# Performance work log

Hardware: AMD Instinct MI355X
Metric: run time of the kernel (lower is better)

Reference implementation:

```python
import jax, jax.numpy as jnp
import numpy as np

HEADS = 16
DIM_HEAD = 64
NPATCH = 256
LN_EPS = 1e-5


def setup_inputs() -> dict:
    key = jax.random.key(0)
    ks = jax.random.split(key, 6)
    B, S, D = 4, 2048, 1024
    inner = HEADS * DIM_HEAD  # 1024
    x = jax.random.normal(ks[0], (B, S, D), dtype=jnp.float32)
    ln_gamma = jnp.ones((D,), dtype=jnp.float32)
    ln_beta = jnp.zeros((D,), dtype=jnp.float32)
    # torch Linear: y = x @ W.T; we store the transposed weight directly.
    Wqkv = jax.random.normal(ks[1], (D, 3 * inner), dtype=jnp.float32) / np.sqrt(D)
    Wout = jax.random.normal(ks[2], (inner, D), dtype=jnp.float32) / np.sqrt(inner)
    bout = jnp.zeros((D,), dtype=jnp.float32)
    return {"x": x, "ln_gamma": ln_gamma, "ln_beta": ln_beta,
            "Wqkv": Wqkv, "Wout": Wout, "bout": bout}


def reference(x, ln_gamma, ln_beta, Wqkv, Wout, bout):
    B, S, D = x.shape
    # LayerNorm
    mu = jnp.mean(x, axis=-1, keepdims=True)
    var = jnp.mean(jnp.square(x - mu), axis=-1, keepdims=True)
    xn = (x - mu) * jax.lax.rsqrt(var + LN_EPS) * ln_gamma + ln_beta
    # QKV projection
    qkv = xn @ Wqkv  # [B, S, 3*H*Dh]
    q, k, v = jnp.split(qkv, 3, axis=-1)
    q = q.reshape(B, S, HEADS, DIM_HEAD)
    k = k.reshape(B, S, HEADS, DIM_HEAD)
    v = v.reshape(B, S, HEADS, DIM_HEAD)
    scale = DIM_HEAD ** -0.5
    dots = jnp.einsum('bqhd,bkhd->bhqk', q, k) * scale  # [B,H,S,S]
    # block-causal mask: query window i attends to key windows 0..i
    win = jnp.arange(S) // NPATCH
    mask = win[:, None] >= win[None, :]  # [S, S] bool
    dots = jnp.where(mask[None, None], dots, -jnp.inf)
    attn = jax.nn.softmax(dots, axis=-1)
    out = jnp.einsum('bhqk,bkhd->bqhd', attn, v).reshape(B, S, HEADS * DIM_HEAD)
    return out @ Wout + bout
```

## Files before the change

### kernel.cpp

```cpp
#include <hip/hip_runtime.h>
#include <stdint.h>

typedef unsigned short u16;
typedef __attribute__((ext_vector_type(8))) short bf16x8;
typedef __attribute__((ext_vector_type(4))) float f32x4;
typedef __attribute__((ext_vector_type(4))) unsigned short u16x4;
typedef __attribute__((ext_vector_type(4))) unsigned int u32x4;

#define DEVI static __device__ __forceinline__

#define QSCALE (0.125f * 1.4426950408889634f)

DEVI u16 f2bf(float f) {
  union { float f; unsigned int u; } v; v.f = f;
  unsigned int u = v.u + 0x7fffu + ((v.u >> 16) & 1u);
  return (u16)(u >> 16);
}
DEVI void gl16(const void* g, void* l) {
  __builtin_amdgcn_global_load_lds(
      (__attribute__((address_space(1))) void*)g,
      (__attribute__((address_space(3))) void*)l, 16, 0, 0);
}
DEVI unsigned int cvtpk(float a, float b) {
  unsigned int r;
  asm("v_cvt_pk_bf16_f32 %0, %1, %2" : "=v"(r) : "v"(a), "v"(b));
  return r;
}
DEVI float fexp2(float x) {
  float r;
  asm("v_exp_f32 %0, %1\n\ts_nop 0" : "=v"(r) : "v"(x));
  return r;
}
DEVI float fmax4(f32x4 v) {
  return fmaxf(fmaxf(v[0], v[1]), fmaxf(v[2], v[3]));
}

__global__ __launch_bounds__(256) void k_ln_split(
    const float* __restrict__ x, const float* __restrict__ gamma,
    const float* __restrict__ beta, u16* __restrict__ xh) {
  const int row = blockIdx.x;
  const int t = threadIdx.x;
  const float4* xr = (const float4*)(x + (size_t)row * 1024);
  float4 v = xr[t];
  float s = v.x + v.y + v.z + v.w;
  float s2 = v.x * v.x + v.y * v.y + v.z * v.z + v.w * v.w;
  #pragma unroll
  for (int m = 1; m < 64; m <<= 1) { s += __shfl_xor(s, m); s2 += __shfl_xor(s2, m); }
  __shared__ float ls[4], ls2[4];
  if ((t & 63) == 0) { ls[t >> 6] = s; ls2[t >> 6] = s2; }
  __syncthreads();
  s = ls[0] + ls[1] + ls[2] + ls[3];
  s2 = ls2[0] + ls2[1] + ls2[2] + ls2[3];
  float mu = s * (1.0f / 1024.0f);
  float var = s2 * (1.0f / 1024.0f) - mu * mu;
  float rstd = rsqrtf(var + 1e-5f);
  float4 g = ((const float4*)gamma)[t];
  float4 b = ((const float4*)beta)[t];
  float xv[4] = {v.x, v.y, v.z, v.w};
  float gg[4] = {g.x, g.y, g.z, g.w};
  float bb[4] = {b.x, b.y, b.z, b.w};
  u16x4 hv;
  #pragma unroll
  for (int i = 0; i < 4; i++) {
    float xn = (xv[i] - mu) * rstd * gg[i] + bb[i];
    hv[i] = f2bf(xn);
  }
  ((u16x4*)xh)[(size_t)row * 256 + t] = hv;
}

__global__ __launch_bounds__(256) void k_wsplit_t(
    const float* __restrict__ W, u16* __restrict__ Wth, int K, int N) {
  __shared__ float tile[32][33];
  const int t = threadIdx.x;
  const int tx = t & 31, ty = t >> 5;
  #pragma unroll
  for (int i = 0; i < 4; i++) {
    int k = blockIdx.y * 32 + ty + i * 8;
    int n = blockIdx.x * 32 + tx;
    tile[ty + i * 8][tx] = W[(size_t)k * N + n];
  }
  __syncthreads();
  #pragma unroll
  for (int i = 0; i < 4; i++) {
    int n = blockIdx.x * 32 + ty + i * 8;
    int k = blockIdx.y * 32 + tx;
    Wth[(size_t)n * K + k] = f2bf(tile[tx][ty + i * 8]);
  }
}

__global__ __launch_bounds__(512, 2) void k_gemmq(
    const u16* __restrict__ Ah, const u16* __restrict__ Bh,
    u16* __restrict__ Qh, u16* __restrict__ Kh, u16* __restrict__ Vth) {
  __shared__ u16 sA[2][256 * 64];
  __shared__ u16 sB[2][256 * 64];
  const int t = threadIdx.x, lane = t & 63, w = t >> 6;
  const int bm = blockIdx.x, bn = blockIdx.y;
  const int wm2 = w >> 2, wn4 = w & 3;
  const int g = lane >> 4, c = lane & 15;
  const size_t arow0 = (size_t)bm * 256, brow0 = (size_t)bn * 256;

  const int sr = t >> 3;
  const int scs = (t & 7) ^ (sr & 7);
  const int brs = (t >> 3) & 31;
  const int bcs = (t & 7) ^ (brs & 7);
  const int bsj = t >> 8;

  f32x4 acc[8][4] = {};

#define STAGE_A(u, kt, b) do { \
    int rA0 = (u) * 64 + sr, rA1 = 128 + rA0; \
    gl16(Ah + (arow0 + rA0) * 1024 + (size_t)(kt) * 64 + scs * 8, \
         sA[b] + (size_t)((u) * 512 + t) * 8); \
    gl16(Ah + (arow0 + rA1) * 1024 + (size_t)(kt) * 64 + scs * 8, \
         sA[b] + (size_t)(1024 + (u) * 512 + t) * 8); \
  } while (0)
#define STAGE_B(u, kt, b) do { \
    int s0_ = bsj, s1_ = bsj + 2; \
    int rB0 = (u) * 32 + s0_ * 64 + brs, rB1 = (u) * 32 + s1_ * 64 + brs; \
    gl16(Bh + (brow0 + rB0) * 1024 + (size_t)(kt) * 64 + bcs * 8, \
         sB[b] + (size_t)(rB0 * 8 + (t & 7)) * 8); \
    gl16(Bh + (brow0 + rB1) * 1024 + (size_t)(kt) * 64 + bcs * 8, \
         sB[b] + (size_t)(rB1 * 8 + (t & 7)) * 8); \
  } while (0)
#define PWAIT_V(tail) do { \
    if (tail) asm volatile("s_waitcnt vmcnt(0)" ::: "memory"); \
    else      asm volatile("s_waitcnt vmcnt(6)" ::: "memory"); \
    __builtin_amdgcn_s_barrier(); \
    asm volatile("s_waitcnt lgkmcnt(0)" ::: "memory"); \
  } while (0)
#define PWAIT_N() do { \
    __builtin_amdgcn_s_barrier(); \
    asm volatile("s_waitcnt lgkmcnt(0)" ::: "memory"); \
  } while (0)

  STAGE_A(0, 0, 0); STAGE_B(0, 0, 0);
  STAGE_A(1, 0, 0); STAGE_B(1, 0, 0);
  STAGE_A(0, 1, 1); STAGE_B(0, 1, 1);
  PWAIT_V(0);

  bf16x8 af[8], bf0[4], bf1[4];
  for (int kt = 0; kt < 16; kt++) {
    const int cur = kt & 1;
    const int tail = (kt >= 14);
    const u16* A_ = sA[cur];
    const u16* B_ = sB[cur];

    #pragma unroll
    for (int mi = 0; mi < 4; mi++)
      #pragma unroll
      for (int ks = 0; ks < 2; ks++) {
        int row = wm2 * 128 + mi * 16 + c;
        af[mi * 2 + ks] = *(const bf16x8*)(A_ + row * 64 + (((ks * 4 + g) ^ (row & 7)) * 8));
      }
    #pragma unroll
    for (int ni = 0; ni < 2; ni++)
      #pragma unroll
      for (int ks = 0; ks < 2; ks++) {
        int row = wn4 * 64 + ni * 16 + c;
        bf0[ni * 2 + ks] = *(const bf16x8*)(B_ + row * 64 + (((ks * 4 + g) ^ (row & 7)) * 8));
      }
    if (kt + 1 < 16) STAGE_A(1, kt + 1, (kt + 1) & 1);
    PWAIT_V(tail);
    __builtin_amdgcn_s_setprio(1);
    #pragma unroll
    for (int mi = 0; mi < 4; mi++)
      #pragma unroll
      for (int ni = 0; ni < 2; ni++)
        #pragma unroll
        for (int ks = 0; ks < 2; ks++)
          acc[mi][ni] = __builtin_amdgcn_mfma_f32_16x16x32_bf16(af[mi * 2 + ks], bf0[ni * 2 + ks], acc[mi][ni], 0, 0, 0);
    __builtin_amdgcn_s_setprio(0);

    #pragma unroll
    for (int ni = 0; ni < 2; ni++)
      #pragma unroll
      for (int ks = 0; ks < 2; ks++) {
        int row = wn4 * 64 + 32 + ni * 16 + c;
        bf1[ni * 2 + ks] = *(const bf16x8*)(B_ + row * 64 + (((ks * 4 + g) ^ (row & 7)) * 8));
      }
    if (kt + 1 < 16) STAGE_B(1, kt + 1, (kt + 1) & 1);
    PWAIT_N();
    __builtin_amdgcn_s_setprio(1);
    #pragma unroll
    for (int mi = 0; mi < 4; mi++)
      #pragma unroll
      for (int ni = 0; ni < 2; ni++)
        #pragma unroll
        for (int ks = 0; ks < 2; ks++)
          acc[mi][2 + ni] = __builtin_amdgcn_mfma_f32_16x16x32_bf16(af[mi * 2 + ks], bf1[ni * 2 + ks], acc[mi][2 + ni], 0, 0, 0);
    __builtin_amdgcn_s_setprio(0);

    #pragma unroll
    for (int mi = 0; mi < 4; mi++)
      #pragma unroll
      for (int ks = 0; ks < 2; ks++) {
        int row = wm2 * 128 + 64 + mi * 16 + c;
        af[mi * 2 + ks] = *(const bf16x8*)(A_ + row * 64 + (((ks * 4 + g) ^ (row & 7)) * 8));
      }
    if (kt + 2 < 16) STAGE_A(0, kt + 2, cur);
    PWAIT_N();
    __builtin_amdgcn_s_setprio(1);
    #pragma unroll
    for (int mi = 0; mi < 4; mi++)
      #pragma unroll
      for (int ni = 0; ni < 2; ni++)
        #pragma unroll
        for (int ks = 0; ks < 2; ks++)
          acc[4 + mi][ni] = __builtin_amdgcn_mfma_f32_16x16x32_bf16(af[mi * 2 + ks], bf0[ni * 2 + ks], acc[4 + mi][ni], 0, 0, 0);
    __builtin_amdgcn_s_setprio(0);

    if (kt + 2 < 16) STAGE_B(0, kt + 2, cur);
    PWAIT_N();
    __builtin_amdgcn_s_setprio(1);
    #pragma unroll
    for (int mi = 0; mi < 4; mi++)
      #pragma unroll
      for (int ni = 0; ni < 2; ni++)
        #pragma unroll
        for (int ks = 0; ks < 2; ks++)
          acc[4 + mi][2 + ni] = __builtin_amdgcn_mfma_f32_16x16x32_bf16(af[mi * 2 + ks], bf1[ni * 2 + ks], acc[4 + mi][2 + ni], 0, 0, 0);
    __builtin_amdgcn_s_setprio(0);
  }

  #pragma unroll
  for (int am = 0; am < 8; am++) {
    int grow0 = bm * 256 + wm2 * 128 + (am >> 2) * 64 + (am & 3) * 16 + g * 4;
    int b = grow0 >> 11, s0 = grow0 & 2047;
    #pragma unroll
    for (int an = 0; an < 4; an++) {
      int gcol = bn * 256 + wn4 * 64 + (an >> 1) * 32 + (an & 1) * 16 + c;
      int which = gcol >> 10, rem = gcol & 1023;
      int hh = rem >> 6, dd = rem & 63;
      if (which == 2) {
        u16x4 hv;
        #pragma unroll
        for (int r = 0; r < 4; r++) hv[r] = f2bf(acc[am][an][r]);
        size_t off = ((size_t)((b * 16 + hh) * 64 + dd)) * 2048 + s0;
        *(u16x4*)(Vth + off) = hv;
      } else {
        u16* dh = which ? Kh : Qh;
        float sc = which ? 1.0f : QSCALE;
        #pragma unroll
        for (int r = 0; r < 4; r++) {
          size_t off = ((size_t)(b * 16 + hh) * 2048 + (s0 + r)) * 64 + dd;
          dh[off] = f2bf(acc[am][an][r] * sc);
        }
      }
    }
  }
#undef STAGE_A
#undef STAGE_B
#undef PWAIT_V
#undef PWAIT_N
}

__global__ __launch_bounds__(256) void k_gemmo(
    const u16* __restrict__ Ah, const u16* __restrict__ Bh,
    float* __restrict__ Cout, const float* __restrict__ bias) {
  __shared__ u16 sA[2][128 * 64];
  __shared__ u16 sB[2][128 * 64];
  const int t = threadIdx.x, lane = t & 63, w = t >> 6;
  const int bm = blockIdx.x, bn = blockIdx.y;
  const int wm = (w >> 1) * 64, wn = (w & 1) * 64;
  const int g = lane >> 4, c = lane & 15;
  const size_t arow0 = (size_t)bm * 128, brow0 = (size_t)bn * 128;

  const int r0 = t >> 3, cc0 = t & 7;
  const int cs0 = cc0 ^ (r0 & 7);
  const u16* gA = Ah + (arow0 + r0) * 1024 + cs0 * 8;
  const u16* gB = Bh + (brow0 + r0) * 1024 + cs0 * 8;

  f32x4 acc[4][4] = {};

  #pragma unroll
  for (int i = 0; i < 4; i++) {
    gl16(gA + (size_t)i * 32768, sA[0] + (size_t)(t + i * 256) * 8);
    gl16(gB + (size_t)i * 32768, sB[0] + (size_t)(t + i * 256) * 8);
  }
  gA += 64; gB += 64;
  __syncthreads();

  for (int kt = 0; kt < 16; kt++) {
    const int cur = kt & 1, nxt = cur ^ 1;
    if (kt + 1 < 16) {
      #pragma unroll
      for (int i = 0; i < 4; i++) {
        gl16(gA + (size_t)i * 32768, sA[nxt] + (size_t)(t + i * 256) * 8);
        gl16(gB + (size_t)i * 32768, sB[nxt] + (size_t)(t + i * 256) * 8);
      }
      gA += 64; gB += 64;
    }
    #pragma unroll
    for (int ks = 0; ks < 2; ks++) {
      bf16x8 afh[4], bfh[4];
      #pragma unroll
      for (int mi = 0; mi < 4; mi++) {
        int row = wm + mi * 16 + c;
        afh[mi] = *(const bf16x8*)(sA[cur] + row * 64 + (((ks * 4 + g) ^ (row & 7)) * 8));
      }
      #pragma unroll
      for (int ni = 0; ni < 4; ni++) {
        int row = wn + ni * 16 + c;
        bfh[ni] = *(const bf16x8*)(sB[cur] + row * 64 + (((ks * 4 + g) ^ (row & 7)) * 8));
      }
      #pragma unroll
      for (int mi = 0; mi < 4; mi++)
        #pragma unroll
        for (int ni = 0; ni < 4; ni++)
          acc[mi][ni] = __builtin_amdgcn_mfma_f32_16x16x32_bf16(afh[mi], bfh[ni], acc[mi][ni], 0, 0, 0);
    }
    __syncthreads();
  }

  #pragma unroll
  for (int mi = 0; mi < 4; mi++) {
    int grow0 = bm * 128 + wm + mi * 16 + g * 4;
    #pragma unroll
    for (int ni = 0; ni < 4; ni++) {
      int gcol = bn * 128 + wn + ni * 16 + c;
      float bb = bias[gcol];
      #pragma unroll
      for (int r = 0; r < 4; r++)
        Cout[(size_t)(grow0 + r) * 1024 + gcol] = acc[mi][ni][r] + bb;
    }
  }
}

__global__ __launch_bounds__(512, 4) void k_attn(
    const u16* __restrict__ Qh, const u16* __restrict__ Kh,
    const u16* __restrict__ Vth, u16* __restrict__ Oh) {
  __shared__ u16 lK[2][128 * 64], lV[2][64 * 128];
  const int t = threadIdx.x, lane = t & 63, w = t >> 6;
  const int bh = blockIdx.x;
  const int qt = 15 - blockIdx.y;
  const int b = bh >> 4, h = bh & 15;
  const int qrow0 = qt * 128;
  const int kvlen = (qt / 2 + 1) * 256;
  const int g = lane >> 4, c = lane & 15;

  bf16x8 qf[2];
  {
    const u16* qb = Qh + ((size_t)bh * 2048 + qrow0 + w * 16) * 64;
    #pragma unroll
    for (int ks = 0; ks < 2; ks++)
      qf[ks] = *(const bf16x8*)(qb + (size_t)c * 64 + ks * 32 + g * 8);
  }

  const u16* Kb = Kh + (size_t)bh * 2048 * 64;
  const u16* Vb = Vth + (size_t)bh * 64 * 2048;

  int kbase[2], vbase[4];
  #pragma unroll
  for (int ks = 0; ks < 2; ks++) kbase[ks] = c * 64 + (((ks * 4 + g) ^ (c & 7)) * 8);
  #pragma unroll
  for (int ks = 0; ks < 4; ks++) vbase[ks] = c * 128 + (((ks * 4 + g) ^ c) * 8);

  const int kr0 = t >> 3, kcs0 = (t & 7) ^ (kr0 & 7);
  const int vr0 = t >> 4, vcs0 = (t & 15) ^ (vr0 & 15);

  const bf16x8 vones = {(short)0x3F80, (short)0x3F80, (short)0x3F80, (short)0x3F80,
                        (short)0x3F80, (short)0x3F80, (short)0x3F80, (short)0x3F80};

  float mrun = 0.f;
  f32x4 lsum = {0.f, 0.f, 0.f, 0.f};
  f32x4 o[4] = {};

  const int ntiles = kvlen >> 7;

  gl16(Kb + (size_t)kr0 * 64 + kcs0 * 8, lK[0] + (size_t)t * 8);
  gl16(Kb + (size_t)(kr0 + 64) * 64 + kcs0 * 8, lK[0] + (size_t)(t + 512) * 8);
  gl16(Vb + (size_t)vr0 * 2048 + vcs0 * 8, lV[0] + (size_t)t * 8);
  gl16(Vb + (size_t)(vr0 + 32) * 2048 + vcs0 * 8, lV[0] + (size_t)(t + 512) * 8);
  __syncthreads();

  const u16* gK = Kb + (size_t)(128 + kr0) * 64 + kcs0 * 8;
  const u16* gV = Vb + (size_t)vr0 * 2048 + 128 + vcs0 * 8;

  for (int kt = 0; kt < ntiles; kt++) {
    const int cur = kt & 1, nxt = cur ^ 1;
    if (kt + 1 < ntiles) {
      gl16(gK, lK[nxt] + (size_t)t * 8);
      gl16(gK + 64 * 64, lK[nxt] + (size_t)(t + 512) * 8);
      gl16(gV, lV[nxt] + (size_t)t * 8);
      gl16(gV + 32 * 2048, lV[nxt] + (size_t)(t + 512) * 8);
      gK += 128 * 64;  gV += 128;
    }

    f32x4 s[8];
    #pragma unroll
    for (int ni = 0; ni < 8; ni++)
      s[ni] = (f32x4){-mrun, -mrun, -mrun, -mrun};
    __builtin_amdgcn_s_setprio(1);
    #pragma unroll
    for (int ni = 0; ni < 8; ni++)
      #pragma unroll
      for (int ks = 0; ks < 2; ks++) {
        bf16x8 kf = *(const bf16x8*)(lK[cur] + ni * 1024 + kbase[ks]);
        s[ni] = __builtin_amdgcn_mfma_f32_16x16x32_bf16(kf, qf[ks], s[ni], 0, 0, 0);
      }
    __builtin_amdgcn_s_setprio(0);

    float tl = fmaxf(fmaxf(fmaxf(fmax4(s[0]), fmax4(s[1])), fmaxf(fmax4(s[2]), fmax4(s[3]))),
                     fmaxf(fmaxf(fmax4(s[4]), fmax4(s[5])), fmaxf(fmax4(s[6]), fmax4(s[7]))));
    if (!__all(tl <= 8.0f)) {
      float tm = fmaxf(tl, __shfl_xor(tl, 16));
      tm = fmaxf(tm, __shfl_xor(tm, 32));
      float delta = fmaxf(tm, 0.0f);
      mrun += delta;
      float al = fexp2(-delta);
      #pragma unroll
      for (int ni = 0; ni < 8; ni++)
        #pragma unroll
        for (int r = 0; r < 4; r++) s[ni][r] -= delta;
      #pragma unroll
      for (int r = 0; r < 4; r++) {
        float ar = __shfl(al, g * 4 + r);
        lsum[r] *= ar;
        #pragma unroll
        for (int di = 0; di < 4; di++) o[di][r] *= ar;
      }
    }

    bf16x8 pa[4];
    #pragma unroll
    for (int ks = 0; ks < 4; ks++) {
      unsigned int e0 = cvtpk(fexp2(s[2 * ks][0]), fexp2(s[2 * ks][1]));
      unsigned int e1 = cvtpk(fexp2(s[2 * ks][2]), fexp2(s[2 * ks][3]));
      unsigned int f0 = cvtpk(fexp2(s[2 * ks + 1][0]), fexp2(s[2 * ks + 1][1]));
      unsigned int f1 = cvtpk(fexp2(s[2 * ks + 1][2]), fexp2(s[2 * ks + 1][3]));
      asm volatile("v_permlane32_swap_b32 %0, %1" : "+v"(e0), "+v"(f0));
      asm volatile("v_permlane16_swap_b32 %0, %1" : "+v"(e0), "+v"(f0));
      asm volatile("v_permlane32_swap_b32 %0, %1" : "+v"(e1), "+v"(f1));
      asm volatile("v_permlane16_swap_b32 %0, %1" : "+v"(e1), "+v"(f1));
      union { u32x4 u; bf16x8 bv; } cvu;
      cvu.u = (u32x4){e0, e1, f0, f1};
      pa[ks] = cvu.bv;
    }

    __builtin_amdgcn_s_setprio(1);
    #pragma unroll
    for (int di = 0; di < 4; di++)
      #pragma unroll
      for (int ks = 0; ks < 4; ks++) {
        bf16x8 vf = *(const bf16x8*)(lV[cur] + di * 2048 + vbase[ks]);
        o[di] = __builtin_amdgcn_mfma_f32_16x16x32_bf16(pa[ks], vf, o[di], 0, 0, 0);
      }
    #pragma unroll
    for (int ks = 0; ks < 4; ks++)
      lsum = __builtin_amdgcn_mfma_f32_16x16x32_bf16(pa[ks], vones, lsum, 0, 0, 0);
    __builtin_amdgcn_s_setprio(0);

    __syncthreads();
  }

  #pragma unroll
  for (int r = 0; r < 4; r++) {
    float ir = 1.0f / lsum[r];
    int srow = qrow0 + w * 16 + g * 4 + r;
    size_t rowo = ((size_t)b * 2048 + srow) * 1024 + h * 64;
    #pragma unroll
    for (int di = 0; di < 4; di++)
      Oh[rowo + di * 16 + c] = f2bf(o[di][r] * ir);
  }
}

extern "C" void kernel_launch(void* const* d_in, const int* in_sizes, int n_in,
                              void* d_out, int out_size, void* d_ws, size_t ws_size,
                              hipStream_t stream) {
  const float* x     = (const float*)d_in[0];
  const float* gamma = (const float*)d_in[1];
  const float* beta  = (const float*)d_in[2];
  const float* Wqkv  = (const float*)d_in[3];
  const float* Wout  = (const float*)d_in[4];
  const float* bout  = (const float*)d_in[5];
  float* out = (float*)d_out;

  char* ws = (char*)d_ws;
  size_t off = 0;
  auto alloc = [&](size_t bytes) { char* p = ws + off; off += (bytes + 255) & ~(size_t)255; return p; };
  const size_t SZ_XN = (size_t)8192 * 1024 * 2;
  const size_t SZ_WQ = (size_t)3072 * 1024 * 2;
  const size_t SZ_WO = (size_t)1024 * 1024 * 2;
  const size_t SZ_QKV = (size_t)4 * 16 * 2048 * 64 * 2;
  u16* xnh  = (u16*)alloc(SZ_XN);
  u16* wqth = (u16*)alloc(SZ_WQ);
  u16* woth = (u16*)alloc(SZ_WO);
  u16* Qh  = (u16*)alloc(SZ_QKV);
  u16* Kh  = (u16*)alloc(SZ_QKV);
  u16* Vth = (u16*)alloc(SZ_QKV);
  if (off > ws_size) return;

  k_ln_split<<<8192, 256, 0, stream>>>(x, gamma, beta, xnh);
  k_wsplit_t<<<dim3(96, 32), 256, 0, stream>>>(Wqkv, wqth, 1024, 3072);
  k_wsplit_t<<<dim3(32, 32), 256, 0, stream>>>(Wout, woth, 1024, 1024);
  k_gemmq<<<dim3(32, 12), 512, 0, stream>>>(xnh, wqth, Qh, Kh, Vth);
  k_attn<<<dim3(64, 16), 512, 0, stream>>>(Qh, Kh, Vth, xnh);
  k_gemmo<<<dim3(64, 8), 256, 0, stream>>>(xnh, woth, out, bout);
}
```

Baseline: 158.4 us.

## Split V projection out of QKV GEMM into separate templated GEMM kernel

The QKV GEMM now computes only Q and K (grid 32x8), and V is computed by a separate 128x128-tile GEMM kernel that writes the transposed V layout directly. The output-projection GEMM is folded into the same template, and its LDS double buffering is replaced by a single buffer with synchronisation before and after each load. The likely intent is to remove the divergent V-transpose epilogue from the large GEMM and improve grid balance. In exchange it adds a kernel launch, and dropping double buffering exposes global-load latency in both the V and output GEMMs.

```diff
diff --git a/kernel.cpp b/kernel.cpp
--- a/kernel.cpp
+++ b/kernel.cpp
@@ -90,7 +90,7 @@
 
 __global__ __launch_bounds__(512, 2) void k_gemmq(
     const u16* __restrict__ Ah, const u16* __restrict__ Bh,
-    u16* __restrict__ Qh, u16* __restrict__ Kh, u16* __restrict__ Vth) {
+    u16* __restrict__ Qh, u16* __restrict__ Kh) {
   __shared__ u16 sA[2][256 * 64];
   __shared__ u16 sB[2][256 * 64];
   const int t = threadIdx.x, lane = t & 63, w = t >> 6;
@@ -231,20 +231,12 @@
       int gcol = bn * 256 + wn4 * 64 + (an >> 1) * 32 + (an & 1) * 16 + c;
       int which = gcol >> 10, rem = gcol & 1023;
       int hh = rem >> 6, dd = rem & 63;
-      if (which == 2) {
-        u16x4 hv;
-        #pragma unroll
-        for (int r = 0; r < 4; r++) hv[r] = f2bf(acc[am][an][r]);
-        size_t off = ((size_t)((b * 16 + hh) * 64 + dd)) * 2048 + s0;
-        *(u16x4*)(Vth + off) = hv;
-      } else {
-        u16* dh = which ? Kh : Qh;
-        float sc = which ? 1.0f : QSCALE;
-        #pragma unroll
-        for (int r = 0; r < 4; r++) {
-          size_t off = ((size_t)(b * 16 + hh) * 2048 + (s0 + r)) * 64 + dd;
-          dh[off] = f2bf(acc[am][an][r] * sc);
-        }
+      u16* dh = which ? Kh : Qh;
+      float sc = which ? 1.0f : QSCALE;
+      #pragma unroll
+      for (int r = 0; r < 4; r++) {
+        size_t off = ((size_t)(b * 16 + hh) * 2048 + (s0 + r)) * 64 + dd;
+        dh[off] = f2bf(acc[am][an][r] * sc);
       }
     }
   }
@@ -254,54 +246,45 @@
 #undef PWAIT_N
 }
 
-__global__ __launch_bounds__(256) void k_gemmo(
+template <int MODE>
+__global__ __launch_bounds__(256) void k_gemm2(
     const u16* __restrict__ Ah, const u16* __restrict__ Bh,
-    float* __restrict__ Cout, const float* __restrict__ bias) {
-  __shared__ u16 sA[2][128 * 64];
-  __shared__ u16 sB[2][128 * 64];
+    u16* __restrict__ Vth, float* __restrict__ Cout,
+    const float* __restrict__ bias) {
+  __shared__ u16 sA[128 * 64];
+  __shared__ u16 sB[128 * 64];
   const int t = threadIdx.x, lane = t & 63, w = t >> 6;
   const int bm = blockIdx.x, bn = blockIdx.y;
   const int wm = (w >> 1) * 64, wn = (w & 1) * 64;
   const int g = lane >> 4, c = lane & 15;
   const size_t arow0 = (size_t)bm * 128, brow0 = (size_t)bn * 128;
 
-  const int r0 = t >> 3, cc0 = t & 7;
-  const int cs0 = cc0 ^ (r0 & 7);
-  const u16* gA = Ah + (arow0 + r0) * 1024 + cs0 * 8;
-  const u16* gB = Bh + (brow0 + r0) * 1024 + cs0 * 8;
-
   f32x4 acc[4][4] = {};
 
-  #pragma unroll
-  for (int i = 0; i < 4; i++) {
-    gl16(gA + (size_t)i * 32768, sA[0] + (size_t)(t + i * 256) * 8);
-    gl16(gB + (size_t)i * 32768, sB[0] + (size_t)(t + i * 256) * 8);
-  }
-  gA += 64; gB += 64;
-  __syncthreads();
-
   for (int kt = 0; kt < 16; kt++) {
-    const int cur = kt & 1, nxt = cur ^ 1;
-    if (kt + 1 < 16) {
-      #pragma unroll
-      for (int i = 0; i < 4; i++) {
-        gl16(gA + (size_t)i * 32768, sA[nxt] + (size_t)(t + i * 256) * 8);
-        gl16(gB + (size_t)i * 32768, sB[nxt] + (size_t)(t + i * 256) * 8);
-      }
-      gA += 64; gB += 64;
-    }
+    __syncthreads();
+    #pragma unroll
+    for (int i = 0; i < 4; i++) {
+      int ci = t + i * 256;
+      int r = ci >> 3, cc = ci & 7;
+      int cs = cc ^ (r & 7);
+      size_t ka = (size_t)kt * 64 + cs * 8;
+      gl16(Ah + (arow0 + r) * 1024 + ka, sA + (size_t)ci * 8);
+      gl16(Bh + (brow0 + r) * 1024 + ka, sB + (size_t)ci * 8);
+    }
+    __syncthreads();
     #pragma unroll
     for (int ks = 0; ks < 2; ks++) {
       bf16x8 afh[4], bfh[4];
       #pragma unroll
       for (int mi = 0; mi < 4; mi++) {
         int row = wm + mi * 16 + c;
-        afh[mi] = *(const bf16x8*)(sA[cur] + row * 64 + (((ks * 4 + g) ^ (row & 7)) * 8));
+        afh[mi] = *(const bf16x8*)(sA + row * 64 + (((ks * 4 + g) ^ (row & 7)) * 8));
       }
       #pragma unroll
       for (int ni = 0; ni < 4; ni++) {
         int row = wn + ni * 16 + c;
-        bfh[ni] = *(const bf16x8*)(sB[cur] + row * 64 + (((ks * 4 + g) ^ (row & 7)) * 8));
+        bfh[ni] = *(const bf16x8*)(sB + row * 64 + (((ks * 4 + g) ^ (row & 7)) * 8));
       }
       #pragma unroll
       for (int mi = 0; mi < 4; mi++)
@@ -309,19 +292,36 @@
         for (int ni = 0; ni < 4; ni++)
           acc[mi][ni] = __builtin_amdgcn_mfma_f32_16x16x32_bf16(afh[mi], bfh[ni], acc[mi][ni], 0, 0, 0);
     }
-    __syncthreads();
-  }
-
-  #pragma unroll
-  for (int mi = 0; mi < 4; mi++) {
-    int grow0 = bm * 128 + wm + mi * 16 + g * 4;
-    #pragma unroll
-    for (int ni = 0; ni < 4; ni++) {
-      int gcol = bn * 128 + wn + ni * 16 + c;
-      float bb = bias[gcol];
-      #pragma unroll
-      for (int r = 0; r < 4; r++)
-        Cout[(size_t)(grow0 + r) * 1024 + gcol] = acc[mi][ni][r] + bb;
+  }
+
+  if (MODE == 2) {
+    #pragma unroll
+    for (int mi = 0; mi < 4; mi++) {
+      int grow0 = bm * 128 + wm + mi * 16 + g * 4;
+      int b = grow0 >> 11, s0 = grow0 & 2047;
+      #pragma unroll
+      for (int ni = 0; ni < 4; ni++) {
+        int vcol = bn * 128 + wn + ni * 16 + c;
+        int hh = vcol >> 6, dd = vcol & 63;
+        u16x4 hv;
+        #pragma unroll
+        for (int r = 0; r < 4; r++) hv[r] = f2bf(acc[mi][ni][r]);
+        size_t off = ((size_t)((b * 16 + hh) * 64 + dd)) * 2048 + s0;
+        *(u16x4*)(Vth + off) = hv;
+      }
+    }
+  } else {
+    #pragma unroll
+    for (int mi = 0; mi < 4; mi++) {
+      int grow0 = bm * 128 + wm + mi * 16 + g * 4;
+      #pragma unroll
+      for (int ni = 0; ni < 4; ni++) {
+        int gcol = bn * 128 + wn + ni * 16 + c;
+        float bb = bias[gcol];
+        #pragma unroll
+        for (int r = 0; r < 4; r++)
+          Cout[(size_t)(grow0 + r) * 1024 + gcol] = acc[mi][ni][r] + bb;
+      }
     }
   }
 }
@@ -493,7 +493,10 @@
   k_ln_split<<<8192, 256, 0, stream>>>(x, gamma, beta, xnh);
   k_wsplit_t<<<dim3(96, 32), 256, 0, stream>>>(Wqkv, wqth, 1024, 3072);
   k_wsplit_t<<<dim3(32, 32), 256, 0, stream>>>(Wout, woth, 1024, 1024);
-  k_gemmq<<<dim3(32, 12), 512, 0, stream>>>(xnh, wqth, Qh, Kh, Vth);
+  k_gemmq<<<dim3(32, 8), 512, 0, stream>>>(xnh, wqth, Qh, Kh);
+  k_gemm2<2><<<dim3(64, 8), 256, 0, stream>>>(xnh, wqth + (size_t)2048 * 1024,
+                                              Vth, nullptr, nullptr);
   k_attn<<<dim3(64, 16), 512, 0, stream>>>(Qh, Kh, Vth, xnh);
-  k_gemmo<<<dim3(64, 8), 256, 0, stream>>>(xnh, woth, out, bout);
-}
+  k_gemm2<1><<<dim3(64, 8), 256, 0, stream>>>(xnh, woth,
+                                              nullptr, out, bout);
+}
```

After: 155.9 us. No clear change (-1.6%).
